# Optimization experiments

Measured on AMD Instinct MI355X. Metric: run time of the kernel, lower is better.

Reference implementation:

```python
import jax, jax.numpy as jnp
import numpy as np

B, S, D, H = 2, 2048, 768, 12
DH = D // H


def setup_inputs() -> dict:
    key = jax.random.key(0)
    ks = jax.random.split(key, 12)
    f32 = jnp.float32
    sd = 1.0 / np.sqrt(D)
    return {
        "q": jax.random.normal(ks[0], (B, S, D), f32),
        "k": jax.random.normal(ks[1], (B, S, D), f32),
        "v": jax.random.normal(ks[2], (B, S, D), f32),
        "mask": jax.random.normal(ks[3], (S, S), f32),
        "Wq": jax.random.normal(ks[4], (D, D), f32) * sd,
        "bq": jnp.zeros((D,), f32),
        "Wk": jax.random.normal(ks[5], (D, D), f32) * sd,
        "bk": jnp.zeros((D,), f32),
        "Wv": jax.random.normal(ks[6], (D, D), f32) * sd,
        "bv": jnp.zeros((D,), f32),
        "Wo": jax.random.normal(ks[7], (D, D), f32) * sd,
        "bo": jnp.zeros((D,), f32),
    }


def reference(q, k, v, mask, Wq, bq, Wk, bk, Wv, bv, Wo, bo):
    # torch nn.Linear: y = x @ W.T + b
    qh = (q @ Wq.T + bq).reshape(B, S, H, DH).transpose(0, 2, 1, 3)  # [B,H,S,DH]
    kh = (k @ Wk.T + bk).reshape(B, S, H, DH).transpose(0, 2, 1, 3)
    vh = (v @ Wv.T + bv).reshape(B, S, H, DH).transpose(0, 2, 1, 3)
    scores = jnp.einsum("bhsd,bhtd->bhst", qh, kh)  # [B,H,S,S]
    # original adds mask after permute to [H,B,S,S]; with an [S,S] mask the
    # broadcast add is identical either way
    scores = scores + mask
    attn = jax.nn.softmax(scores.astype(jnp.float32) / np.sqrt(DH), axis=-1)
    out = jnp.einsum("bhst,bhtd->bhsd", attn, vh)  # [B,H,S,DH]
    out = out.transpose(0, 2, 1, 3).reshape(B, S, D)
    return out @ Wo.T + bo
```

## Files before the change

kernel.cpp:

```cpp
#include <hip/hip_runtime.h>
#include <hip/hip_bf16.h>

#define B_ 2
#define S_ 2048
#define D_ 768
#define H_ 12
#define DH_ 64
#define M_ (B_*S_)
#define BH_ (B_*H_)

typedef __bf16 v8bf __attribute__((ext_vector_type(8)));
typedef __bf16 v4bf __attribute__((ext_vector_type(4)));
typedef float  v4f  __attribute__((ext_vector_type(4)));

static __device__ __forceinline__ v4f mfma16(v8bf a, v8bf b, v4f c) {
  return __builtin_amdgcn_mfma_f32_16x16x32_bf16(a, b, c, 0, 0, 0);
}

static __device__ __forceinline__ void gload_lds16(const __bf16* g, __bf16* l) {
  __builtin_amdgcn_global_load_lds(
      (const __attribute__((address_space(1))) unsigned int*)g,
      (__attribute__((address_space(3))) unsigned int*)l,
      16, 0, 0);
}

#define C1_ 0.18033688011112042f

__global__ __launch_bounds__(256) void convert_kernel(
    const float* __restrict__ q, const float* __restrict__ k, const float* __restrict__ v,
    const float* __restrict__ Wq, const float* __restrict__ Wk,
    const float* __restrict__ Wv, const float* __restrict__ Wo,
    __bf16* __restrict__ Xq, __bf16* __restrict__ Xk, __bf16* __restrict__ Xv,
    __bf16* __restrict__ Wqb, __bf16* __restrict__ Wkb,
    __bf16* __restrict__ Wvb, __bf16* __restrict__ Wob)
{
  const float* src; __bf16* dst; int n;
  switch (blockIdx.y) {
    case 0: src = q;  dst = Xq;  n = M_*D_; break;
    case 1: src = k;  dst = Xk;  n = M_*D_; break;
    case 2: src = v;  dst = Xv;  n = M_*D_; break;
    case 3: src = Wq; dst = Wqb; n = D_*D_; break;
    case 4: src = Wk; dst = Wkb; n = D_*D_; break;
    case 5: src = Wv; dst = Wvb; n = D_*D_; break;
    default: src = Wo; dst = Wob; n = D_*D_; break;
  }
  int n4 = n >> 2;
  for (int i = blockIdx.x*blockDim.x + threadIdx.x; i < n4; i += gridDim.x*blockDim.x) {
    float4 x = ((const float4*)src)[i];
    v4bf y;
    y[0] = (__bf16)x.x; y[1] = (__bf16)x.y; y[2] = (__bf16)x.z; y[3] = (__bf16)x.w;
    ((v4bf*)dst)[i] = y;
  }
}

__global__ __launch_bounds__(256) void em_kernel(
    const float* __restrict__ mask, __bf16* __restrict__ em)
{
  int t = blockIdx.x*256 + threadIdx.x;
  int L = t & 63; int rest = t >> 6;
  int half = rest & 1; rest >>= 1;
  int qq = rest & 3; rest >>= 2;
  int ktile = rest & 63; rest >>= 6;
  int qt = rest;
  int row = qt*64 + qq*16 + (L & 15);
  int key0 = ktile*32 + half*16 + ((L >> 4) << 2);
  const float* mp = mask + (size_t)row*S_ + key0;
  float4 m4 = *(const float4*)mp;
  v4bf e;
  e[0] = (__bf16)exp2f(C1_*m4.x); e[1] = (__bf16)exp2f(C1_*m4.y);
  e[2] = (__bf16)exp2f(C1_*m4.z); e[3] = (__bf16)exp2f(C1_*m4.w);
  *(v4bf*)(em + (size_t)t*4) = e;
}

template<int BM, int BN>
static __device__ __forceinline__ void gemm_core_lds(
    const __bf16* __restrict__ A, const __bf16* __restrict__ W,
    int m0, int n0, __bf16* lds, v4f acc[BM/32][BN/32])
{
  constexpr int NFA = BM/16, NFB = BN/16;
  constexpr int PW  = (NFA + NFB) / 4;
  constexpr int MI  = BM/32, NJ = BN/32;
  const int lane = threadIdx.x & 63;
  const int wave = threadIdx.x >> 6;
  const int r16 = lane & 15;
  const int kc8 = (lane >> 4) << 3;
  const int ia = (wave >> 1) * MI;
  const int ib = (wave & 1) * NJ;

  const __bf16* gsrc[PW]; __bf16* ldst[PW];
  #pragma unroll
  for (int t = 0; t < PW; t++) {
    int fb = wave*PW + t;
    gsrc[t] = (fb < NFA)
        ? A + (size_t)(m0 + fb*16 + r16)*D_ + kc8
        : W + (size_t)(n0 + (fb - NFA)*16 + r16)*D_ + kc8;
    ldst[t] = lds + fb*512;
  }

  for (int k0 = 0; k0 < D_; k0 += 32) {
    #pragma unroll
    for (int t = 0; t < PW; t++) gload_lds16(gsrc[t] + k0, ldst[t]);
    __syncthreads();
    v8bf a[MI], b[NJ];
    #pragma unroll
    for (int i = 0; i < MI; i++) a[i] = *(const v8bf*)(lds + (ia+i)*512 + lane*8);
    #pragma unroll
    for (int j = 0; j < NJ; j++) b[j] = *(const v8bf*)(lds + (NFA+ib+j)*512 + lane*8);
    #pragma unroll
    for (int i = 0; i < MI; i++)
      #pragma unroll
      for (int j = 0; j < NJ; j++)
        acc[i][j] = mfma16(a[i], b[j], acc[i][j]);
    __syncthreads();
  }
}

__global__ __launch_bounds__(256) void qkv_gemm(
    const __bf16* __restrict__ Xq, const __bf16* __restrict__ Xk, const __bf16* __restrict__ Xv,
    const __bf16* __restrict__ Wqb, const __bf16* __restrict__ Wkb, const __bf16* __restrict__ Wvb,
    const float* __restrict__ bq, const float* __restrict__ bk, const float* __restrict__ bv,
    __bf16* __restrict__ qf, __bf16* __restrict__ kf, __bf16* __restrict__ vf)
{
  __shared__ __bf16 lds[(128+64)*32];
  const int mode = blockIdx.z;
  const __bf16* A = (mode == 0) ? Xq : (mode == 1) ? Xk : Xv;
  const __bf16* W = (mode == 0) ? Wqb : (mode == 1) ? Wkb : Wvb;
  const float* bias = (mode == 0) ? bq : (mode == 1) ? bk : bv;
  const int m0 = blockIdx.y << 7, n0 = blockIdx.x << 6;
  v4f acc[4][2];
  #pragma unroll
  for (int i = 0; i < 4; i++)
    #pragma unroll
    for (int j = 0; j < 2; j++) { v4f z = {0.f,0.f,0.f,0.f}; acc[i][j] = z; }
  gemm_core_lds<128,64>(A, W, m0, n0, lds, acc);

  const int lane = threadIdx.x & 63;
  const int wave = threadIdx.x >> 6;
  const int wm = (wave >> 1) << 6, wn = (wave & 1) << 5;
  const int col = lane & 15, quad = lane >> 4;
  float bb[2]; int nn[2];
  #pragma unroll
  for (int j = 0; j < 2; j++) { nn[j] = n0 + wn + 16*j + col; bb[j] = bias[nn[j]]; }

  if (mode < 2) {
    __bf16* dst = (mode == 0) ? qf : kf;
    #pragma unroll
    for (int i = 0; i < 4; i++)
      #pragma unroll
      for (int r = 0; r < 4; r++) {
        int m = m0 + wm + 16*i + quad*4 + r;
        int batch = m >> 11, s = m & (S_-1);
        #pragma unroll
        for (int j = 0; j < 2; j++) {
          int n = nn[j];
          int h = n >> 6, dd = n & 63;
          size_t flat = (((size_t)(batch*H_ + h)*128 + (s >> 4))*2 + (dd >> 5))*512
                      + ((((dd >> 3) & 3)*16 + (s & 15)) << 3) + (dd & 7);
          dst[flat] = (__bf16)(acc[i][j][r] + bb[j]);
        }
      }
  } else {
    #pragma unroll
    for (int i = 0; i < 4; i++) {
      int mbase = m0 + wm + 16*i + quad*4;
      int batch = mbase >> 11, s0 = mbase & (S_-1);
      #pragma unroll
      for (int j = 0; j < 2; j++) {
        int n = nn[j];
        int h = n >> 6, dd = n & 63;
        v4bf pk;
        #pragma unroll
        for (int r = 0; r < 4; r++) pk[r] = (__bf16)(acc[i][j][r] + bb[j]);
        size_t flat = (((size_t)(batch*H_ + h)*64 + (s0 >> 5))*4 + (dd >> 4))*512
                    + ((((s0 >> 3) & 3)*16 + (dd & 15)) << 3) + (s0 & 7);
        *(v4bf*)(vf + flat) = pk;
      }
    }
  }
}

__global__ __launch_bounds__(256) void attn_kernel(
    const __bf16* __restrict__ qf, const __bf16* __restrict__ kf, const __bf16* __restrict__ vf,
    const __bf16* __restrict__ em, __bf16* __restrict__ ao)
{
  __shared__ __bf16 plds[4][4][16][40];
  __shared__ float ls[4][64];
  __shared__ float Ored[64][68];

  const int bh = blockIdx.y;
  const int wave = threadIdx.x >> 6, lane = threadIdx.x & 63;
  const int col = lane & 15, quad = lane >> 4, koff = quad << 3;
  const int q0 = blockIdx.x << 6;
  const int batch = bh / H_, h = bh % H_;
  const __bf16* qfb = qf + (size_t)bh * (S_*DH_);
  const __bf16* kfb = kf + (size_t)bh * (S_*DH_);
  const __bf16* vfb = vf + (size_t)bh * (S_*DH_);
  const __bf16* emb = em + (size_t)(q0 >> 6) * 131072;
  __bf16 (*pt)[16][40] = plds[wave];

  v8bf Qf[4][2];
  #pragma unroll
  for (int qq = 0; qq < 4; qq++) {
    const __bf16* qblk = qfb + (size_t)((q0 >> 4) + qq)*1024;
    Qf[qq][0] = *(const v8bf*)(qblk + lane*8);
    Qf[qq][1] = *(const v8bf*)(qblk + 512 + lane*8);
  }

  v4f O[4][4];
  #pragma unroll
  for (int f = 0; f < 4; f++)
    #pragma unroll
    for (int qq = 0; qq < 4; qq++) { v4f z = {0.f,0.f,0.f,0.f}; O[f][qq] = z; }
  float li[4];
  #pragma unroll
  for (int qq = 0; qq < 4; qq++) li[qq] = 0.f;

  const int kbeg = wave << 9;
  #pragma unroll 1
  for (int kt = kbeg; kt < kbeg + 512; kt += 32) {
    const __bf16* kblk = kfb + (size_t)(kt >> 4)*1024;
    v8bf Kf00 = *(const v8bf*)(kblk + lane*8);
    v8bf Kf01 = *(const v8bf*)(kblk + 512 + lane*8);
    v8bf Kf10 = *(const v8bf*)(kblk + 1024 + lane*8);
    v8bf Kf11 = *(const v8bf*)(kblk + 1536 + lane*8);
    const __bf16* eblk = emb + (size_t)(kt >> 5)*2048;

    #pragma unroll
    for (int qq = 0; qq < 4; qq++) {
      v4f s0 = {0.f,0.f,0.f,0.f}, s1 = {0.f,0.f,0.f,0.f};
      s0 = mfma16(Kf00, Qf[qq][0], s0); s0 = mfma16(Kf01, Qf[qq][1], s0);
      s1 = mfma16(Kf10, Qf[qq][0], s1); s1 = mfma16(Kf11, Qf[qq][1], s1);
      v4bf e0 = *(const v4bf*)(eblk + qq*512 + lane*4);
      v4bf e1 = *(const v4bf*)(eblk + qq*512 + 256 + lane*4);

      float p[8], rs = 0.f;
      #pragma unroll
      for (int j = 0; j < 4; j++) {
        p[j]   = exp2f(s0[j]*C1_) * (float)e0[j];
        p[4+j] = exp2f(s1[j]*C1_) * (float)e1[j];
      }
      #pragma unroll
      for (int j = 0; j < 8; j++) rs += p[j];
      li[qq] += rs;
      v4bf pk0, pk1;
      #pragma unroll
      for (int r = 0; r < 4; r++) { pk0[r] = (__bf16)p[r]; pk1[r] = (__bf16)p[4+r]; }
      *(v4bf*)(&pt[qq][col][quad*4])      = pk0;
      *(v4bf*)(&pt[qq][col][16 + quad*4]) = pk1;
    }

    const __bf16* vblk = vfb + (size_t)(kt >> 5)*2048;
    v8bf Pf[4];
    #pragma unroll
    for (int qq = 0; qq < 4; qq++) Pf[qq] = *(const v8bf*)(&pt[qq][col][koff]);
    #pragma unroll
    for (int f = 0; f < 4; f++) {
      v8bf Vf = *(const v8bf*)(vblk + f*512 + lane*8);
      #pragma unroll
      for (int qq = 0; qq < 4; qq++)
        O[f][qq] = mfma16(Vf, Pf[qq], O[f][qq]);
    }
  }

  #pragma unroll
  for (int qq = 0; qq < 4; qq++) {
    float rs = li[qq];
    rs += __shfl_xor(rs, 16);
    rs += __shfl_xor(rs, 32);
    if (quad == 0) ls[wave][16*qq + col] = rs;
  }
  __syncthreads();

  for (int w = 0; w < 4; w++) {
    if (wave == w) {
      #pragma unroll
      for (int qq = 0; qq < 4; qq++)
        #pragma unroll
        for (int f = 0; f < 4; f++) {
          float4* dst = (float4*)&Ored[16*qq + col][16*f + quad*4];
          float4 val;
          val.x = O[f][qq][0]; val.y = O[f][qq][1];
          val.z = O[f][qq][2]; val.w = O[f][qq][3];
          if (w != 0) {
            float4 old = *dst;
            val.x += old.x; val.y += old.y; val.z += old.z; val.w += old.w;
          }
          *dst = val;
        }
    }
    __syncthreads();
  }
  {
    int q = threadIdx.x >> 2, ds = (threadIdx.x & 3) << 4;
    float lst = ls[0][q] + ls[1][q] + ls[2][q] + ls[3][q];
    float invl = 1.f / lst;
    __bf16* orow = ao + ((size_t)batch*S_ + q0 + q)*D_ + h*DH_ + ds;
    v8bf o0, o1;
    #pragma unroll
    for (int i = 0; i < 8; i++) {
      o0[i] = (__bf16)(Ored[q][ds + i] * invl);
      o1[i] = (__bf16)(Ored[q][ds + 8 + i] * invl);
    }
    *(v8bf*)orow = o0;
    *(v8bf*)(orow + 8) = o1;
  }
}

__global__ __launch_bounds__(256) void out_gemm(
    const __bf16* __restrict__ Ao, const __bf16* __restrict__ Wob,
    const float* __restrict__ bo, float* __restrict__ out)
{
  __shared__ __bf16 lds[(64+64)*32];
  const int m0 = blockIdx.y << 6, n0 = blockIdx.x << 6;
  v4f acc[2][2];
  #pragma unroll
  for (int i = 0; i < 2; i++)
    #pragma unroll
    for (int j = 0; j < 2; j++) { v4f z = {0.f,0.f,0.f,0.f}; acc[i][j] = z; }
  gemm_core_lds<64,64>(Ao, Wob, m0, n0, lds, acc);

  const int lane = threadIdx.x & 63;
  const int wave = threadIdx.x >> 6;
  const int wm = (wave >> 1) << 5, wn = (wave & 1) << 5;
  const int col = lane & 15, quad = lane >> 4;
  float bb[2]; int nn[2];
  #pragma unroll
  for (int j = 0; j < 2; j++) { nn[j] = n0 + wn + 16*j + col; bb[j] = bo[nn[j]]; }
  #pragma unroll
  for (int i = 0; i < 2; i++)
    #pragma unroll
    for (int r = 0; r < 4; r++) {
      int m = m0 + wm + 16*i + quad*4 + r;
      #pragma unroll
      for (int j = 0; j < 2; j++)
        out[(size_t)m*D_ + nn[j]] = acc[i][j][r] + bb[j];
    }
}

extern "C" void kernel_launch(void* const* d_in, const int* in_sizes, int n_in,
                              void* d_out, int out_size, void* d_ws, size_t ws_size,
                              hipStream_t stream)
{
  const float* q    = (const float*)d_in[0];
  const float* k    = (const float*)d_in[1];
  const float* v    = (const float*)d_in[2];
  const float* mask = (const float*)d_in[3];
  const float* Wq   = (const float*)d_in[4];
  const float* bq   = (const float*)d_in[5];
  const float* Wk   = (const float*)d_in[6];
  const float* bk   = (const float*)d_in[7];
  const float* Wv   = (const float*)d_in[8];
  const float* bv   = (const float*)d_in[9];
  const float* Wo   = (const float*)d_in[10];
  const float* bo   = (const float*)d_in[11];

  const size_t XN = (size_t)M_ * D_;
  const size_t WN = (size_t)D_ * D_;
  const size_t HN = (size_t)BH_ * S_ * DH_;

  char* ws = (char*)d_ws;
  __bf16* Xq  = (__bf16*)ws;                 ws += XN * 2;
  __bf16* Xk  = (__bf16*)ws;                 ws += XN * 2;
  __bf16* Xv  = (__bf16*)ws;                 ws += XN * 2;
  __bf16* Wqb = (__bf16*)ws;                 ws += WN * 2;
  __bf16* Wkb = (__bf16*)ws;                 ws += WN * 2;
  __bf16* Wvb = (__bf16*)ws;                 ws += WN * 2;
  __bf16* Wob = (__bf16*)ws;                 ws += WN * 2;
  __bf16* qfb = (__bf16*)ws;                 ws += HN * 2;
  __bf16* kfb = (__bf16*)ws;                 ws += HN * 2;
  __bf16* vfb = (__bf16*)ws;                 ws += HN * 2;
  __bf16* aob = (__bf16*)ws;                 ws += XN * 2;
  __bf16* emb = Xq;

  convert_kernel<<<dim3(3072, 7), 256, 0, stream>>>(
      q, k, v, Wq, Wk, Wv, Wo, Xq, Xk, Xv, Wqb, Wkb, Wvb, Wob);
  qkv_gemm<<<dim3(12, 32, 3), 256, 0, stream>>>(
      Xq, Xk, Xv, Wqb, Wkb, Wvb, bq, bk, bv, qfb, kfb, vfb);
  em_kernel<<<dim3(4096), 256, 0, stream>>>(mask, emb);
  attn_kernel<<<dim3(32, 24), 256, 0, stream>>>(qfb, kfb, vfb, emb, aob);
  out_gemm<<<dim3(12, 64), 256, 0, stream>>>(aob, Wob, bo, (float*)d_out);
}
```

Before: 282.0 us.

## Prefetch K tiles, fold softmax scale into Q, widen mask-exp loads

The attention loop now double-buffers K fragments in registers, loading the next tile while the current one is consumed, and hoists the V loads to the top of each iteration to hide global latency. The softmax scale is folded into Q at projection time, removing one multiply per score. em_kernel's layout is repacked so each thread writes 8 contiguous bf16 values, letting attention read mask factors with a single 16-byte load, and it launches half as many blocks. Launch bounds request 3 blocks per CU, which may raise register pressure or cause spills because of the extra live K/V fragments. Rounding Q to bf16 after scaling changes the numerics slightly.

Result: no change. 283.6 us (+0.6%).

```diff
diff --git a/kernel.cpp b/kernel.cpp
--- a/kernel.cpp
+++ b/kernel.cpp
@@ -58,18 +58,20 @@
 {
   int t = blockIdx.x*256 + threadIdx.x;
   int L = t & 63; int rest = t >> 6;
-  int half = rest & 1; rest >>= 1;
   int qq = rest & 3; rest >>= 2;
   int ktile = rest & 63; rest >>= 6;
   int qt = rest;
   int row = qt*64 + qq*16 + (L & 15);
-  int key0 = ktile*32 + half*16 + ((L >> 4) << 2);
+  int key0 = ktile*32 + ((L >> 4) << 2);
   const float* mp = mask + (size_t)row*S_ + key0;
-  float4 m4 = *(const float4*)mp;
-  v4bf e;
-  e[0] = (__bf16)exp2f(C1_*m4.x); e[1] = (__bf16)exp2f(C1_*m4.y);
-  e[2] = (__bf16)exp2f(C1_*m4.z); e[3] = (__bf16)exp2f(C1_*m4.w);
-  *(v4bf*)(em + (size_t)t*4) = e;
+  float4 m0 = *(const float4*)mp;
+  float4 m1 = *(const float4*)(mp + 16);
+  v8bf e;
+  e[0] = (__bf16)exp2f(C1_*m0.x); e[1] = (__bf16)exp2f(C1_*m0.y);
+  e[2] = (__bf16)exp2f(C1_*m0.z); e[3] = (__bf16)exp2f(C1_*m0.w);
+  e[4] = (__bf16)exp2f(C1_*m1.x); e[5] = (__bf16)exp2f(C1_*m1.y);
+  e[6] = (__bf16)exp2f(C1_*m1.z); e[7] = (__bf16)exp2f(C1_*m1.w);
+  *(v8bf*)(em + (size_t)t*8) = e;
 }
 
 template<int BM, int BN>
@@ -144,6 +146,7 @@
 
   if (mode < 2) {
     __bf16* dst = (mode == 0) ? qf : kf;
+    const float sc = (mode == 0) ? C1_ : 1.0f;
     #pragma unroll
     for (int i = 0; i < 4; i++)
       #pragma unroll
@@ -156,7 +159,7 @@
           int h = n >> 6, dd = n & 63;
           size_t flat = (((size_t)(batch*H_ + h)*128 + (s >> 4))*2 + (dd >> 5))*512
                       + ((((dd >> 3) & 3)*16 + (s & 15)) << 3) + (dd & 7);
-          dst[flat] = (__bf16)(acc[i][j][r] + bb[j]);
+          dst[flat] = (__bf16)((acc[i][j][r] + bb[j]) * sc);
         }
       }
   } else {
@@ -179,7 +182,7 @@
   }
 }
 
-__global__ __launch_bounds__(256) void attn_kernel(
+__global__ __launch_bounds__(256, 3) void attn_kernel(
     const __bf16* __restrict__ qf, const __bf16* __restrict__ kf, const __bf16* __restrict__ vf,
     const __bf16* __restrict__ em, __bf16* __restrict__ ao)
 {
@@ -216,28 +219,34 @@
   for (int qq = 0; qq < 4; qq++) li[qq] = 0.f;
 
   const int kbeg = wave << 9;
+
+  const __bf16* kblk0 = kfb + (size_t)(kbeg >> 4)*1024;
+  v8bf Ka0 = *(const v8bf*)(kblk0 + lane*8);
+  v8bf Ka1 = *(const v8bf*)(kblk0 + 512 + lane*8);
+  v8bf Ka2 = *(const v8bf*)(kblk0 + 1024 + lane*8);
+  v8bf Ka3 = *(const v8bf*)(kblk0 + 1536 + lane*8);
+
   #pragma unroll 1
   for (int kt = kbeg; kt < kbeg + 512; kt += 32) {
-    const __bf16* kblk = kfb + (size_t)(kt >> 4)*1024;
-    v8bf Kf00 = *(const v8bf*)(kblk + lane*8);
-    v8bf Kf01 = *(const v8bf*)(kblk + 512 + lane*8);
-    v8bf Kf10 = *(const v8bf*)(kblk + 1024 + lane*8);
-    v8bf Kf11 = *(const v8bf*)(kblk + 1536 + lane*8);
+    const __bf16* vblk = vfb + (size_t)(kt >> 5)*2048;
+    v8bf Vf0 = *(const v8bf*)(vblk + lane*8);
+    v8bf Vf1 = *(const v8bf*)(vblk + 512 + lane*8);
+    v8bf Vf2 = *(const v8bf*)(vblk + 1024 + lane*8);
+    v8bf Vf3 = *(const v8bf*)(vblk + 1536 + lane*8);
     const __bf16* eblk = emb + (size_t)(kt >> 5)*2048;
 
     #pragma unroll
     for (int qq = 0; qq < 4; qq++) {
+      v8bf ef = *(const v8bf*)(eblk + qq*512 + lane*8);
       v4f s0 = {0.f,0.f,0.f,0.f}, s1 = {0.f,0.f,0.f,0.f};
-      s0 = mfma16(Kf00, Qf[qq][0], s0); s0 = mfma16(Kf01, Qf[qq][1], s0);
-      s1 = mfma16(Kf10, Qf[qq][0], s1); s1 = mfma16(Kf11, Qf[qq][1], s1);
-      v4bf e0 = *(const v4bf*)(eblk + qq*512 + lane*4);
-      v4bf e1 = *(const v4bf*)(eblk + qq*512 + 256 + lane*4);
+      s0 = mfma16(Ka0, Qf[qq][0], s0); s0 = mfma16(Ka1, Qf[qq][1], s0);
+      s1 = mfma16(Ka2, Qf[qq][0], s1); s1 = mfma16(Ka3, Qf[qq][1], s1);
 
       float p[8], rs = 0.f;
       #pragma unroll
       for (int j = 0; j < 4; j++) {
-        p[j]   = exp2f(s0[j]*C1_) * (float)e0[j];
-        p[4+j] = exp2f(s1[j]*C1_) * (float)e1[j];
+        p[j]   = exp2f(s0[j]) * (float)ef[j];
+        p[4+j] = exp2f(s1[j]) * (float)ef[4+j];
       }
       #pragma unroll
       for (int j = 0; j < 8; j++) rs += p[j];
@@ -249,16 +258,23 @@
       *(v4bf*)(&pt[qq][col][16 + quad*4]) = pk1;
     }
 
-    const __bf16* vblk = vfb + (size_t)(kt >> 5)*2048;
+    if (kt + 32 < kbeg + 512) {
+      const __bf16* nk = kfb + (size_t)((kt + 32) >> 4)*1024;
+      Ka0 = *(const v8bf*)(nk + lane*8);
+      Ka1 = *(const v8bf*)(nk + 512 + lane*8);
+      Ka2 = *(const v8bf*)(nk + 1024 + lane*8);
+      Ka3 = *(const v8bf*)(nk + 1536 + lane*8);
+    }
+
     v8bf Pf[4];
     #pragma unroll
     for (int qq = 0; qq < 4; qq++) Pf[qq] = *(const v8bf*)(&pt[qq][col][koff]);
     #pragma unroll
-    for (int f = 0; f < 4; f++) {
-      v8bf Vf = *(const v8bf*)(vblk + f*512 + lane*8);
-      #pragma unroll
-      for (int qq = 0; qq < 4; qq++)
-        O[f][qq] = mfma16(Vf, Pf[qq], O[f][qq]);
+    for (int qq = 0; qq < 4; qq++) {
+      O[0][qq] = mfma16(Vf0, Pf[qq], O[0][qq]);
+      O[1][qq] = mfma16(Vf1, Pf[qq], O[1][qq]);
+      O[2][qq] = mfma16(Vf2, Pf[qq], O[2][qq]);
+      O[3][qq] = mfma16(Vf3, Pf[qq], O[3][qq]);
     }
   }
 
@@ -376,7 +392,7 @@
       q, k, v, Wq, Wk, Wv, Wo, Xq, Xk, Xv, Wqb, Wkb, Wvb, Wob);
   qkv_gemm<<<dim3(12, 32, 3), 256, 0, stream>>>(
       Xq, Xk, Xv, Wqb, Wkb, Wvb, bq, bk, bv, qfb, kfb, vfb);
-  em_kernel<<<dim3(4096), 256, 0, stream>>>(mask, emb);
+  em_kernel<<<dim3(2048), 256, 0, stream>>>(mask, emb);
   attn_kernel<<<dim3(32, 24), 256, 0, stream>>>(qfb, kfb, vfb, emb, aob);
   out_gemm<<<dim3(12, 64), 256, 0, stream>>>(aob, Wob, bo, (float*)d_out);
 }
```
